# Kernel tuning notes

Hardware: AMD Instinct MI355X
Metric: run time of the kernel (lower is better)

Reference implementation:

```python
import jax, jax.numpy as jnp
import numpy as np

HIDDEN = 128
N_NODES = 100000
N_EDGES = 200000
NEG_SLOPE = 0.01  # torch LeakyReLU default


def setup_inputs() -> dict:
    key = jax.random.key(0)
    ks = jax.random.split(key, 12)
    h = HIDDEN
    lim = 1.0 / np.sqrt(h)
    lim3 = 1.0 / np.sqrt(3 * h)
    u = lambda k, shape, l: jax.random.uniform(k, shape, jnp.float32, -l, l)
    return {
        "x_src": jax.random.normal(ks[0], (N_NODES, h), jnp.float32),
        "x_dst": jax.random.normal(ks[1], (N_NODES, h), jnp.float32),
        "edge_index": jax.random.randint(ks[2], (2, N_EDGES), 0, N_NODES, jnp.int64),
        # parent_encoder Linear(h, h)
        "Wp": u(ks[3], (h, h), lim), "bp": u(ks[4], (h,), lim),
        # child_encoder Linear(h, h)
        "Wc": u(ks[5], (h, h), lim), "bc": u(ks[6], (h,), lim),
        # edge_weight_mlp: Linear(3h, h) -> ReLU -> Linear(h, h)
        "W1": u(ks[7], (h, 3 * h), lim3), "b1": u(ks[8], (h,), lim3),
        "W2": u(ks[9], (h, h), lim), "b2": u(ks[10], (h,), lim),
    }


def reference(x_src, x_dst, edge_index, Wp, bp, Wc, bc, W1, b1, W2, b2):
    # gather node feats per edge  [E, h]
    par = x_src[edge_index[0]]
    cld = x_dst[edge_index[1]]
    # dual encoders: Linear + LeakyReLU (Dropout is identity in eval)
    enc_p = jax.nn.leaky_relu(par @ Wp.T + bp, NEG_SLOPE)
    enc_c = jax.nn.leaky_relu(cld @ Wc.T + bc, NEG_SLOPE)
    diff = jnp.abs(par - cld)
    ef = jnp.concatenate([enc_p, enc_c, diff], axis=-1)  # [E, 3h]
    # edge_weight_mlp
    edge_attr = jax.nn.relu(ef @ W1.T + b1) @ W2.T + b2  # [E, h]
    return edge_attr
```

## Files before the change

kernel.cpp:

```cpp
#include <hip/hip_runtime.h>

typedef unsigned short u16;
typedef __attribute__((ext_vector_type(8))) short v8s;
typedef __attribute__((ext_vector_type(4))) float v4f;
typedef __attribute__((ext_vector_type(4))) float f4;

#define HID 128
#define TM  64
#define SEF_S 260
#define SH_S  132

__device__ __forceinline__ u16 f2b(float f) {
    union { float f; unsigned u; } v; v.f = f;
    unsigned u = v.u;
    u += 0x7fffu + ((u >> 16) & 1u);
    return (u16)(u >> 16);
}

#define MFMA(A, B, C) __builtin_amdgcn_mfma_f32_16x16x32_bf16(A, B, C, 0, 0, 0)

__global__ void cvt_weights(const float* __restrict__ Wp, const float* __restrict__ Wc,
                            const float* __restrict__ W1, const float* __restrict__ W2,
                            u16* __restrict__ dst)
{
    int i = blockIdx.x * 256 + threadIdx.x;
    const float* s; int off;
    if (i < 4096)       { s = Wp; off = 0; }
    else if (i < 8192)  { s = Wc; off = 4096; }
    else if (i < 20480) { s = W1; off = 8192; }
    else                { s = W2; off = 20480; }
    int j = i - off;
    f4 v = ((const f4*)s)[j];
    u16* d = dst + (size_t)i * 4;
    d[0] = f2b(v[0]); d[1] = f2b(v[1]); d[2] = f2b(v[2]); d[3] = f2b(v[3]);
}

__global__ __launch_bounds__(256, 3) void edge_attr_kernel(
    const float* __restrict__ x_src, const float* __restrict__ x_dst,
    const int* __restrict__ ei,
    const u16* __restrict__ wsW,
    const float* __restrict__ bp, const float* __restrict__ bc,
    const float* __restrict__ b1, const float* __restrict__ b2,
    float* __restrict__ out, int E)
{
    __shared__ __align__(16) u16 sEF[TM * SEF_S];
    __shared__ __align__(16) u16 sH [TM * SH_S];

    const u16* wsWp = wsW;
    const u16* wsWc = wsW + 16384;
    const u16* wsW1 = wsW + 32768;
    const u16* wsW2 = wsW + 81920;

    const int t  = threadIdx.x;
    const int l  = t & 63;
    const int e0 = blockIdx.x * TM;

    int eg = e0 + l; if (eg >= E) eg = E - 1;
    const int pidx = ei[eg];
    const int cidx = ei[E + eg];

    const int cg = (t & 15) << 3;
    #pragma unroll
    for (int i = 0; i < 4; ++i) {
        int r = (t >> 4) + i * 16;
        int rl = r & 63;
        int pi = __shfl(pidx, rl);
        int ci = __shfl(cidx, rl);
        const f4* ps = (const f4*)(x_src + (size_t)pi * HID + cg);
        const f4* qs = (const f4*)(x_dst + (size_t)ci * HID + cg);
        f4 p0 = ps[0], p1 = ps[1];
        f4 q0 = qs[0], q1 = qs[1];
        v8s pb, qb, db;
        #pragma unroll
        for (int j = 0; j < 4; ++j) {
            pb[j]     = (short)f2b(p0[j]);
            pb[j + 4] = (short)f2b(p1[j]);
            qb[j]     = (short)f2b(q0[j]);
            qb[j + 4] = (short)f2b(q1[j]);
            db[j]     = (short)f2b(fabsf(p0[j] - q0[j]));
            db[j + 4] = (short)f2b(fabsf(p1[j] - q1[j]));
        }
        *(v8s*)&sEF[r * SEF_S       + cg] = pb;
        *(v8s*)&sEF[r * SEF_S + 128 + cg] = qb;
        *(v8s*)&sH [r * SH_S        + cg] = db;
    }
    __syncthreads();

    const int lane = l;
    const int ln = lane & 15;
    const int lq = lane >> 4;
    const int n0 = (t >> 6) * 32;

    {
        v8s Bp[2][4], Bc[2][4];
        float bpv[2], bcv[2];
        #pragma unroll
        for (int nt = 0; nt < 2; ++nt) {
            int n = n0 + nt * 16 + ln;
            bpv[nt] = bp[n];
            bcv[nt] = bc[n];
            #pragma unroll
            for (int kt = 0; kt < 4; ++kt) {
                Bp[nt][kt] = *(const v8s*)(wsWp + (size_t)n * HID + kt * 32 + lq * 8);
                Bc[nt][kt] = *(const v8s*)(wsWc + (size_t)n * HID + kt * 32 + lq * 8);
            }
        }
        v4f aP[4][2], aC[4][2];
        #pragma unroll
        for (int mt = 0; mt < 4; ++mt)
            #pragma unroll
            for (int nt = 0; nt < 2; ++nt) {
                aP[mt][nt] = (v4f){0.f, 0.f, 0.f, 0.f};
                aC[mt][nt] = (v4f){0.f, 0.f, 0.f, 0.f};
            }
        #pragma unroll
        for (int mt = 0; mt < 4; ++mt) {
            const int rbase = (mt * 16 + ln) * SEF_S + lq * 8;
            v8s A[4];
            #pragma unroll
            for (int kt = 0; kt < 4; ++kt) A[kt] = *(const v8s*)&sEF[rbase + kt * 32];
            #pragma unroll
            for (int nt = 0; nt < 2; ++nt)
                #pragma unroll
                for (int kt = 0; kt < 4; ++kt) aP[mt][nt] = MFMA(A[kt], Bp[nt][kt], aP[mt][nt]);
            #pragma unroll
            for (int kt = 0; kt < 4; ++kt) A[kt] = *(const v8s*)&sEF[rbase + 128 + kt * 32];
            #pragma unroll
            for (int nt = 0; nt < 2; ++nt)
                #pragma unroll
                for (int kt = 0; kt < 4; ++kt) aC[mt][nt] = MFMA(A[kt], Bc[nt][kt], aC[mt][nt]);
        }
        __syncthreads();
        #pragma unroll
        for (int mt = 0; mt < 4; ++mt)
            #pragma unroll
            for (int nt = 0; nt < 2; ++nt)
                #pragma unroll
                for (int rg = 0; rg < 4; ++rg) {
                    int row = mt * 16 + lq * 4 + rg;
                    int col = n0 + nt * 16 + ln;
                    float vp = aP[mt][nt][rg] + bpv[nt];
                    vp = vp > 0.f ? vp : 0.01f * vp;
                    sEF[row * SEF_S + col] = f2b(vp);
                    float vc = aC[mt][nt][rg] + bcv[nt];
                    vc = vc > 0.f ? vc : 0.01f * vc;
                    sEF[row * SEF_S + 128 + col] = f2b(vc);
                }
        __syncthreads();
    }

    {
        float b1v[2];
        #pragma unroll
        for (int nt = 0; nt < 2; ++nt) b1v[nt] = b1[n0 + nt * 16 + ln];
        v4f acc[4][2];
        #pragma unroll
        for (int mt = 0; mt < 4; ++mt)
            #pragma unroll
            for (int nt = 0; nt < 2; ++nt) acc[mt][nt] = (v4f){0.f, 0.f, 0.f, 0.f};
        #pragma unroll
        for (int ktc = 0; ktc < 3; ++ktc) {
            v8s B[2][4];
            #pragma unroll
            for (int nt = 0; nt < 2; ++nt) {
                int n = n0 + nt * 16 + ln;
                #pragma unroll
                for (int k4 = 0; k4 < 4; ++k4)
                    B[nt][k4] = *(const v8s*)(wsW1 + (size_t)n * 384 + ktc * 128 + k4 * 32 + lq * 8);
            }
            const u16* Asrc = (ktc < 2) ? (sEF + ktc * 128) : sH;
            const int  Astr = (ktc < 2) ? SEF_S : SH_S;
            #pragma unroll
            for (int mt = 0; mt < 4; ++mt) {
                const int rbase = (mt * 16 + ln) * Astr + lq * 8;
                v8s A[4];
                #pragma unroll
                for (int k4 = 0; k4 < 4; ++k4) A[k4] = *(const v8s*)&Asrc[rbase + k4 * 32];
                #pragma unroll
                for (int nt = 0; nt < 2; ++nt)
                    #pragma unroll
                    for (int k4 = 0; k4 < 4; ++k4) acc[mt][nt] = MFMA(A[k4], B[nt][k4], acc[mt][nt]);
            }
        }
        __syncthreads();
        #pragma unroll
        for (int mt = 0; mt < 4; ++mt)
            #pragma unroll
            for (int nt = 0; nt < 2; ++nt)
                #pragma unroll
                for (int rg = 0; rg < 4; ++rg) {
                    int row = mt * 16 + lq * 4 + rg;
                    int col = n0 + nt * 16 + ln;
                    float v = acc[mt][nt][rg] + b1v[nt];
                    sH[row * SH_S + col] = f2b(fmaxf(v, 0.f));
                }
        __syncthreads();
    }

    {
        v8s B2[2][4];
        float b2v[2];
        #pragma unroll
        for (int nt = 0; nt < 2; ++nt) {
            int n = n0 + nt * 16 + ln;
            b2v[nt] = b2[n];
            #pragma unroll
            for (int kt = 0; kt < 4; ++kt)
                B2[nt][kt] = *(const v8s*)(wsW2 + (size_t)n * HID + kt * 32 + lq * 8);
        }
        v4f acc[4][2];
        #pragma unroll
        for (int mt = 0; mt < 4; ++mt)
            #pragma unroll
            for (int nt = 0; nt < 2; ++nt) acc[mt][nt] = (v4f){0.f, 0.f, 0.f, 0.f};
        #pragma unroll
        for (int mt = 0; mt < 4; ++mt) {
            const int rbase = (mt * 16 + ln) * SH_S + lq * 8;
            v8s A[4];
            #pragma unroll
            for (int kt = 0; kt < 4; ++kt) A[kt] = *(const v8s*)&sH[rbase + kt * 32];
            #pragma unroll
            for (int nt = 0; nt < 2; ++nt)
                #pragma unroll
                for (int kt = 0; kt < 4; ++kt) acc[mt][nt] = MFMA(A[kt], B2[nt][kt], acc[mt][nt]);
        }
        #pragma unroll
        for (int mt = 0; mt < 4; ++mt)
            #pragma unroll
            for (int nt = 0; nt < 2; ++nt)
                #pragma unroll
                for (int rg = 0; rg < 4; ++rg) {
                    int row = mt * 16 + lq * 4 + rg;
                    int e = e0 + row;
                    if (e < E)
                        out[(size_t)e * HID + n0 + nt * 16 + ln] = acc[mt][nt][rg] + b2v[nt];
                }
    }
}

extern "C" void kernel_launch(void* const* d_in, const int* in_sizes, int n_in,
                              void* d_out, int out_size, void* d_ws, size_t ws_size,
                              hipStream_t stream) {
    const float* x_src = (const float*)d_in[0];
    const float* x_dst = (const float*)d_in[1];
    const int*   ei    = (const int*)d_in[2];
    const float* Wp    = (const float*)d_in[3];
    const float* bp    = (const float*)d_in[4];
    const float* Wc    = (const float*)d_in[5];
    const float* bc    = (const float*)d_in[6];
    const float* W1    = (const float*)d_in[7];
    const float* b1    = (const float*)d_in[8];
    const float* W2    = (const float*)d_in[9];
    const float* b2    = (const float*)d_in[10];
    float* out = (float*)d_out;
    u16* wsW = (u16*)d_ws;

    int E = in_sizes[2] / 2;

    cvt_weights<<<96, 256, 0, stream>>>(Wp, Wc, W1, W2, wsW);

    int blocks = (E + TM - 1) / TM;
    edge_attr_kernel<<<blocks, 256, 0, stream>>>(
        x_src, x_dst, ei, wsW, bp, bc, b1, b2, out, E);
}
```

Before: 300.1 us.

## Make edge kernel persistent and prefetch next tile's gather during MLP

Converts the one-tile-per-block kernel into a persistent grid of up to 512 blocks that loop over edge tiles. Encoder weights and biases are loaded into registers once per block instead of once per tile. The next tile's node-feature gather is issued into registers before the W1 GEMM and written to shared memory afterward, so gather latency overlaps compute. This needs an extra shared buffer for the diff features and more registers, and launch bounds drop from 3 to 2 blocks per SM, which lowers occupancy.

```diff
diff --git a/kernel.cpp b/kernel.cpp
--- a/kernel.cpp
+++ b/kernel.cpp
@@ -8,7 +8,9 @@
 #define HID 128
 #define TM  64
 #define SEF_S 260
+#define SD_S  132
 #define SH_S  132
+#define NBLK  512
 
 __device__ __forceinline__ u16 f2b(float f) {
     union { float f; unsigned u; } v; v.f = f;
@@ -35,7 +37,51 @@
     d[0] = f2b(v[0]); d[1] = f2b(v[1]); d[2] = f2b(v[2]); d[3] = f2b(v[3]);
 }
 
-__global__ __launch_bounds__(256, 3) void edge_attr_kernel(
+__device__ __forceinline__ void gather_issue(const float* __restrict__ xs,
+                                             const float* __restrict__ xd,
+                                             int pI, int cI, int t,
+                                             f4* rp0, f4* rp1, f4* rq0, f4* rq1)
+{
+    const int cg = (t & 15) << 3;
+    #pragma unroll
+    for (int i = 0; i < 4; ++i) {
+        int r = (t >> 4) + i * 16;
+        int pi = __shfl(pI, r);
+        int ci = __shfl(cI, r);
+        const f4* ps = (const f4*)(xs + (size_t)pi * HID + cg);
+        const f4* qs = (const f4*)(xd + (size_t)ci * HID + cg);
+        rp0[i] = ps[0]; rp1[i] = ps[1];
+        rq0[i] = qs[0]; rq1[i] = qs[1];
+    }
+}
+
+__device__ __forceinline__ void gather_store(int t,
+                                             const f4* rp0, const f4* rp1,
+                                             const f4* rq0, const f4* rq1,
+                                             u16* sEF, u16* sD)
+{
+    const int cg = (t & 15) << 3;
+    #pragma unroll
+    for (int i = 0; i < 4; ++i) {
+        int r = (t >> 4) + i * 16;
+        f4 p0 = rp0[i], p1 = rp1[i], q0 = rq0[i], q1 = rq1[i];
+        v8s pb, qb, db;
+        #pragma unroll
+        for (int j = 0; j < 4; ++j) {
+            pb[j]     = (short)f2b(p0[j]);
+            pb[j + 4] = (short)f2b(p1[j]);
+            qb[j]     = (short)f2b(q0[j]);
+            qb[j + 4] = (short)f2b(q1[j]);
+            db[j]     = (short)f2b(fabsf(p0[j] - q0[j]));
+            db[j + 4] = (short)f2b(fabsf(p1[j] - q1[j]));
+        }
+        *(v8s*)&sEF[r * SEF_S       + cg] = pb;
+        *(v8s*)&sEF[r * SEF_S + 128 + cg] = qb;
+        *(v8s*)&sD [r * SD_S        + cg] = db;
+    }
+}
+
+__global__ __launch_bounds__(256, 2) void edge_attr_kernel(
     const float* __restrict__ x_src, const float* __restrict__ x_dst,
     const int* __restrict__ ei,
     const u16* __restrict__ wsW,
@@ -44,6 +90,7 @@
     float* __restrict__ out, int E)
 {
     __shared__ __align__(16) u16 sEF[TM * SEF_S];
+    __shared__ __align__(16) u16 sD [TM * SD_S];
     __shared__ __align__(16) u16 sH [TM * SH_S];
 
     const u16* wsWp = wsW;
@@ -53,58 +100,47 @@
 
     const int t  = threadIdx.x;
     const int l  = t & 63;
-    const int e0 = blockIdx.x * TM;
-
-    int eg = e0 + l; if (eg >= E) eg = E - 1;
-    const int pidx = ei[eg];
-    const int cidx = ei[E + eg];
-
-    const int cg = (t & 15) << 3;
+    const int ln = l & 15;
+    const int lq = l >> 4;
+    const int n0 = (t >> 6) * 32;
+    const int nT = (E + TM - 1) / TM;
+    const int stride = gridDim.x;
+
+    v8s Bp[2][4], Bc[2][4];
+    float bpv[2], bcv[2], b1v[2], b2v[2];
     #pragma unroll
-    for (int i = 0; i < 4; ++i) {
-        int r = (t >> 4) + i * 16;
-        int rl = r & 63;
-        int pi = __shfl(pidx, rl);
-        int ci = __shfl(cidx, rl);
-        const f4* ps = (const f4*)(x_src + (size_t)pi * HID + cg);
-        const f4* qs = (const f4*)(x_dst + (size_t)ci * HID + cg);
-        f4 p0 = ps[0], p1 = ps[1];
-        f4 q0 = qs[0], q1 = qs[1];
-        v8s pb, qb, db;
-        #pragma unroll
-        for (int j = 0; j < 4; ++j) {
-            pb[j]     = (short)f2b(p0[j]);
-            pb[j + 4] = (short)f2b(p1[j]);
-            qb[j]     = (short)f2b(q0[j]);
-            qb[j + 4] = (short)f2b(q1[j]);
-            db[j]     = (short)f2b(fabsf(p0[j] - q0[j]));
-            db[j + 4] = (short)f2b(fabsf(p1[j] - q1[j]));
-        }
-        *(v8s*)&sEF[r * SEF_S       + cg] = pb;
-        *(v8s*)&sEF[r * SEF_S + 128 + cg] = qb;
-        *(v8s*)&sH [r * SH_S        + cg] = db;
+    for (int nt = 0; nt < 2; ++nt) {
+        int n = n0 + nt * 16 + ln;
+        bpv[nt] = bp[n];  bcv[nt] = bc[n];
+        b1v[nt] = b1[n];  b2v[nt] = b2[n];
+        #pragma unroll
+        for (int kt = 0; kt < 4; ++kt) {
+            Bp[nt][kt] = *(const v8s*)(wsWp + (size_t)n * HID + kt * 32 + lq * 8);
+            Bc[nt][kt] = *(const v8s*)(wsWc + (size_t)n * HID + kt * 32 + lq * 8);
+        }
+    }
+
+    int tile = blockIdx.x;
+    if (tile >= nT) return;
+    {
+        int eg = tile * TM + l; if (eg >= E) eg = E - 1;
+        int pI = ei[eg], cI = ei[E + eg];
+        f4 a0[4], a1[4], c0[4], c1[4];
+        gather_issue(x_src, x_dst, pI, cI, t, a0, a1, c0, c1);
+        gather_store(t, a0, a1, c0, c1, sEF, sD);
     }
     __syncthreads();
 
-    const int lane = l;
-    const int ln = lane & 15;
-    const int lq = lane >> 4;
-    const int n0 = (t >> 6) * 32;
-
-    {
-        v8s Bp[2][4], Bc[2][4];
-        float bpv[2], bcv[2];
-        #pragma unroll
-        for (int nt = 0; nt < 2; ++nt) {
-            int n = n0 + nt * 16 + ln;
-            bpv[nt] = bp[n];
-            bcv[nt] = bc[n];
-            #pragma unroll
-            for (int kt = 0; kt < 4; ++kt) {
-                Bp[nt][kt] = *(const v8s*)(wsWp + (size_t)n * HID + kt * 32 + lq * 8);
-                Bc[nt][kt] = *(const v8s*)(wsWc + (size_t)n * HID + kt * 32 + lq * 8);
-            }
-        }
+    for (;;) {
+        const int e0 = tile * TM;
+        const int nextTile = tile + stride;
+        const bool hasNext = nextTile < nT;
+        const int pTile = hasNext ? nextTile : tile;
+
+        int egN = pTile * TM + l; if (egN >= E) egN = E - 1;
+        int pIN = ei[egN];
+        int cIN = ei[E + egN];
+
         v4f aP[4][2], aC[4][2];
         #pragma unroll
         for (int mt = 0; mt < 4; ++mt)
@@ -147,17 +183,15 @@
                     sEF[row * SEF_S + 128 + col] = f2b(vc);
                 }
         __syncthreads();
-    }
-
-    {
-        float b1v[2];
-        #pragma unroll
-        for (int nt = 0; nt < 2; ++nt) b1v[nt] = b1[n0 + nt * 16 + ln];
-        v4f acc[4][2];
+
+        f4 rp0[4], rp1[4], rq0[4], rq1[4];
+        gather_issue(x_src, x_dst, pIN, cIN, t, rp0, rp1, rq0, rq1);
+
+        v4f acc2[4][2];
         #pragma unroll
         for (int mt = 0; mt < 4; ++mt)
             #pragma unroll
-            for (int nt = 0; nt < 2; ++nt) acc[mt][nt] = (v4f){0.f, 0.f, 0.f, 0.f};
+            for (int nt = 0; nt < 2; ++nt) acc2[mt][nt] = (v4f){0.f, 0.f, 0.f, 0.f};
         #pragma unroll
         for (int ktc = 0; ktc < 3; ++ktc) {
             v8s B[2][4];
@@ -168,8 +202,8 @@
                 for (int k4 = 0; k4 < 4; ++k4)
                     B[nt][k4] = *(const v8s*)(wsW1 + (size_t)n * 384 + ktc * 128 + k4 * 32 + lq * 8);
             }
-            const u16* Asrc = (ktc < 2) ? (sEF + ktc * 128) : sH;
-            const int  Astr = (ktc < 2) ? SEF_S : SH_S;
+            const u16* Asrc = (ktc < 2) ? (sEF + ktc * 128) : sD;
+            const int  Astr = (ktc < 2) ? SEF_S : SD_S;
             #pragma unroll
             for (int mt = 0; mt < 4; ++mt) {
                 const int rbase = (mt * 16 + ln) * Astr + lq * 8;
@@ -179,10 +213,13 @@
                 #pragma unroll
                 for (int nt = 0; nt < 2; ++nt)
                     #pragma unroll
-                    for (int k4 = 0; k4 < 4; ++k4) acc[mt][nt] = MFMA(A[k4], B[nt][k4], acc[mt][nt]);
+                    for (int k4 = 0; k4 < 4; ++k4) acc2[mt][nt] = MFMA(A[k4], B[nt][k4], acc2[mt][nt]);
             }
         }
         __syncthreads();
+
+        gather_store(t, rp0, rp1, rq0, rq1, sEF, sD);
+
         #pragma unroll
         for (int mt = 0; mt < 4; ++mt)
             #pragma unroll
@@ -191,50 +228,50 @@
                 for (int rg = 0; rg < 4; ++rg) {
                     int row = mt * 16 + lq * 4 + rg;
                     int col = n0 + nt * 16 + ln;
-                    float v = acc[mt][nt][rg] + b1v[nt];
+                    float v = acc2[mt][nt][rg] + b1v[nt];
                     sH[row * SH_S + col] = f2b(fmaxf(v, 0.f));
                 }
         __syncthreads();
-    }
-
-    {
-        v8s B2[2][4];
-        float b2v[2];
-        #pragma unroll
-        for (int nt = 0; nt < 2; ++nt) {
-            int n = n0 + nt * 16 + ln;
-            b2v[nt] = b2[n];
-            #pragma unroll
-            for (int kt = 0; kt < 4; ++kt)
-                B2[nt][kt] = *(const v8s*)(wsW2 + (size_t)n * HID + kt * 32 + lq * 8);
-        }
-        v4f acc[4][2];
-        #pragma unroll
-        for (int mt = 0; mt < 4; ++mt)
-            #pragma unroll
-            for (int nt = 0; nt < 2; ++nt) acc[mt][nt] = (v4f){0.f, 0.f, 0.f, 0.f};
-        #pragma unroll
-        for (int mt = 0; mt < 4; ++mt) {
-            const int rbase = (mt * 16 + ln) * SH_S + lq * 8;
-            v8s A[4];
-            #pragma unroll
-            for (int kt = 0; kt < 4; ++kt) A[kt] = *(const v8s*)&sH[rbase + kt * 32];
-            #pragma unroll
-            for (int nt = 0; nt < 2; ++nt)
-                #pragma unroll
-                for (int kt = 0; kt < 4; ++kt) acc[mt][nt] = MFMA(A[kt], B2[nt][kt], acc[mt][nt]);
-        }
-        #pragma unroll
-        for (int mt = 0; mt < 4; ++mt)
-            #pragma unroll
-            for (int nt = 0; nt < 2; ++nt)
-                #pragma unroll
-                for (int rg = 0; rg < 4; ++rg) {
-                    int row = mt * 16 + lq * 4 + rg;
-                    int e = e0 + row;
-                    if (e < E)
-                        out[(size_t)e * HID + n0 + nt * 16 + ln] = acc[mt][nt][rg] + b2v[nt];
-                }
+
+        {
+            v8s B2[2][4];
+            #pragma unroll
+            for (int nt = 0; nt < 2; ++nt) {
+                int n = n0 + nt * 16 + ln;
+                #pragma unroll
+                for (int kt = 0; kt < 4; ++kt)
+                    B2[nt][kt] = *(const v8s*)(wsW2 + (size_t)n * HID + kt * 32 + lq * 8);
+            }
+            v4f acc3[4][2];
+            #pragma unroll
+            for (int mt = 0; mt < 4; ++mt)
+                #pragma unroll
+                for (int nt = 0; nt < 2; ++nt) acc3[mt][nt] = (v4f){0.f, 0.f, 0.f, 0.f};
+            #pragma unroll
+            for (int mt = 0; mt < 4; ++mt) {
+                const int rbase = (mt * 16 + ln) * SH_S + lq * 8;
+                v8s A[4];
+                #pragma unroll
+                for (int kt = 0; kt < 4; ++kt) A[kt] = *(const v8s*)&sH[rbase + kt * 32];
+                #pragma unroll
+                for (int nt = 0; nt < 2; ++nt)
+                    #pragma unroll
+                    for (int kt = 0; kt < 4; ++kt) acc3[mt][nt] = MFMA(A[kt], B2[nt][kt], acc3[mt][nt]);
+            }
+            #pragma unroll
+            for (int mt = 0; mt < 4; ++mt)
+                #pragma unroll
+                for (int nt = 0; nt < 2; ++nt)
+                    #pragma unroll
+                    for (int rg = 0; rg < 4; ++rg) {
+                        int row = mt * 16 + lq * 4 + rg;
+                        int e = e0 + row;
+                        if (e < E)
+                            out[(size_t)e * HID + n0 + nt * 16 + ln] = acc3[mt][nt][rg] + b2v[nt];
+                    }
+        }
+        if (!hasNext) break;
+        tile = nextTile;
     }
 }
 
@@ -256,10 +293,11 @@
     u16* wsW = (u16*)d_ws;
 
     int E = in_sizes[2] / 2;
+    int nT = (E + TM - 1) / TM;
+    int blocks = nT < NBLK ? nT : NBLK;
 
     cvt_weights<<<96, 256, 0, stream>>>(Wp, Wc, W1, W2, wsW);
 
-    int blocks = (E + TM - 1) / TM;
     edge_attr_kernel<<<blocks, 256, 0, stream>>>(
         x_src, x_dst, ei, wsW, bp, bc, b1, b2, out, E);
 }
```

After: 326.6 us. 1.09x slower.
